# Kernel optimization log

Measured on AMD Instinct MI355X. Metric: run time of the kernel, lower is better.

## Reference

```python
import jax, jax.numpy as jnp
import numpy as np

N_FFT = 2048
HOP = 512
OUT_CH = N_FFT // 2 + 1  # 1025


def _dft_conv_weights():
    # periodic ('fftbins=True') Hann window, win_length == n_fft so no padding
    n = np.arange(N_FFT)
    window = 0.5 - 0.5 * np.cos(2.0 * np.pi * n / N_FFT)
    k = np.arange(OUT_CH)
    ang = 2.0 * np.pi * np.outer(k, n) / N_FFT  # (OUT_CH, N_FFT)
    w_real = (np.cos(ang) * window[None, :]).astype(np.float32)
    w_imag = (-np.sin(ang) * window[None, :]).astype(np.float32)
    return jnp.asarray(w_real), jnp.asarray(w_imag)


def setup_inputs() -> dict:
    key = jax.random.key(0)
    x = jax.random.normal(key, (32, 2, 160000), dtype=jnp.float32)
    W_real, W_imag = _dft_conv_weights()
    return {"x": x, "W_real": W_real, "W_imag": W_imag}


def reference(x, W_real, W_imag):
    # x: (B, C, L). center=True -> reflect pad by n_fft//2 on both sides.
    pad = N_FFT // 2
    x_pad = jnp.pad(x, ((0, 0), (0, 0), (pad, pad)), mode="reflect")
    L = x_pad.shape[-1]
    num_frames = (L - N_FFT) // HOP + 1  # 313
    # frame indices: (T, N_FFT)
    idx = jnp.arange(num_frames)[:, None] * HOP + jnp.arange(N_FFT)[None, :]
    frames = x_pad[..., idx]  # (B, C, T, N_FFT)
    # windowed DFT as matmul (equivalent to the Conv1d with stride=hop)
    real = jnp.einsum("bctn,kn->bctk", frames, W_real)
    imag = jnp.einsum("bctn,kn->bctk", frames, W_imag)
    return real, imag
```

## Files before the change

### kernel.cpp

```cpp
#include <hip/hip_runtime.h>

#define B_     32
#define C_     2
#define L_     160000
#define HOP    512
#define PAD    1024
#define LPAD   162048
#define T_     313
#define BC     64
#define M_     20032
#define KCH    1025
#define OUT_HALF 20532800UL
#define PL     81024
#define KD     1024
#define ND     1024
#define NKT    32
#define MT     157
#define NTD    8
#define NWG    1256
#define LIMW   8336

typedef __attribute__((ext_vector_type(8))) short short8;
typedef __attribute__((ext_vector_type(4))) float f32x4;

static __device__ __forceinline__ short f2bf(float f) {
  union { float f; unsigned u; } v; v.f = f;
  unsigned u = v.u;
  unsigned r = (u + 0x7fffu + ((u >> 16) & 1u)) >> 16;
  return (short)r;
}

__global__ void prep_planes(const float* __restrict__ x,
                            short* __restrict__ pl0, short* __restrict__ pl1) {
  int v = blockIdx.x * 256 + threadIdx.x;
  int bc = v / 10128;
  int r  = v - bc * 10128;
  int p0 = r * 8;
  const float* src = x + (size_t)bc * L_;
  short8 e, o;
  if (r >= 64 && r <= 10000) {
    int j0 = 16 * r - 1024;
    #pragma unroll
    for (int qq = 0; qq < 4; ++qq) {
      float4 f = *(const float4*)(src + j0 + qq * 4);
      e[qq * 2 + 0] = f2bf(f.x); o[qq * 2 + 0] = f2bf(f.y);
      e[qq * 2 + 1] = f2bf(f.z); o[qq * 2 + 1] = f2bf(f.w);
    }
  } else {
    #pragma unroll
    for (int u = 0; u < 16; ++u) {
      int j = 16 * r + u - 1024;
      j = j < 0 ? -j : j;
      j = j >= L_ ? 2 * L_ - 2 - j : j;
      short b = f2bf(src[j]);
      if (u & 1) o[u >> 1] = b; else e[u >> 1] = b;
    }
  }
  *(short8*)&pl0[(size_t)bc * PL + p0] = e;
  *(short8*)&pl1[(size_t)bc * PL + p0] = o;
}

__global__ void prep_wb(short* __restrict__ wb0, short* __restrict__ wb1) {
  int id = blockIdx.x * 256 + threadIdx.x;
  int s   = id >> 17;
  int row = (id >> 7) & 1023;
  int n8  = (id & 127) * 8;
  int kp  = row >> 1, e = row & 1;
  short8 ov;
  #pragma unroll
  for (int u = 0; u < 8; ++u) {
    int n1 = n8 + u;
    float win = 0.5f - 0.5f * cosf((float)(2 * n1 + s) * 3.0679615757712823e-3f);
    float tw;
    if (e == 0)       tw = cosf((float)((n1 * kp) & 1023) * 6.1359231515425649e-3f);
    else if (kp == 0) tw = (n1 & 1) ? -1.0f : 1.0f;
    else              tw = -sinf((float)((n1 * kp) & 1023) * 6.1359231515425649e-3f);
    ov[u] = f2bf(win * tw);
  }
  short* wb = s ? wb1 : wb0;
  *(short8*)&wb[(size_t)row * KD + n8] = ov;
}

#define GLOAD16(g, l) __builtin_amdgcn_global_load_lds(                        \
    (const __attribute__((address_space(1))) void*)(g),                        \
    (__attribute__((address_space(3))) void*)(l), 16, 0, 0)

__global__ __launch_bounds__(256, 2) void stft_gemm(const short* __restrict__ pl0,
                                                    const short* __restrict__ pl1,
                                                    const short* __restrict__ wb0,
                                                    const short* __restrict__ wb1,
                                                    float* __restrict__ out) {
  __shared__ __align__(16) char lds[66688];
  const int tid  = threadIdx.x;
  const int lane = tid & 63;
  const int wid  = tid >> 6;

  const int nt = blockIdx.x & 7;
  const int mt = blockIdx.x >> 3;
  const int M0 = mt * 128, N0 = nt * 128;

  const int chunkSwz = ((tid & 3) ^ ((tid >> 3) & 3)) * 8;
  const short* aP[2][2];
  const short* bP[2][2];
  #pragma unroll
  for (int j = 0; j < 2; ++j) {
    int row = j * 64 + (tid >> 2);
    int m = M0 + row; if (m > M_ - 1) m = M_ - 1;
    int bc = m / T_;
    int t  = m - bc * T_;
    size_t base = (size_t)bc * PL + (size_t)t * 256 + chunkSwz;
    aP[0][j] = pl0 + base;
    aP[1][j] = pl1 + base;
    size_t bb = (size_t)(N0 + row) * KD + chunkSwz;
    bP[0][j] = wb0 + bb;
    bP[1][j] = wb1 + bb;
  }
  const int dst[2] = { 0 * 4096 + tid * 16, 1 * 4096 + tid * 16 };

  const int wr = wid >> 1, wc = wid & 1;
  const int fr = lane & 15;
  const int xorb = ((lane >> 4) * 16) ^ ((fr & 6) << 3);
  int afOff[2][4], bfOff[2][4];
  #pragma unroll
  for (int i = 0; i < 4; ++i) {
    afOff[0][i] = (wr * 64 + i * 16 + fr) * 64 + xorb;
    afOff[1][i] = 8192 + (wr * 64 + i * 16 + fr) * 64 + xorb;
    bfOff[0][i] = 16384 + (wc * 64 + i * 16 + fr) * 64 + xorb;
    bfOff[1][i] = 24576 + (wc * 64 + i * 16 + fr) * 64 + xorb;
  }

  f32x4 acc[2][4][4];
  #pragma unroll
  for (int s = 0; s < 2; ++s)
    #pragma unroll
    for (int i = 0; i < 4; ++i)
      #pragma unroll
      for (int j = 0; j < 4; ++j) acc[s][i][j] = (f32x4){0.f, 0.f, 0.f, 0.f};

  {
    char* buf = lds;
    GLOAD16(aP[0][0], buf + dst[0]);
    GLOAD16(aP[0][1], buf + dst[1]);
    GLOAD16(bP[0][0], buf + 16384 + dst[0]);
    GLOAD16(bP[0][1], buf + 16384 + dst[1]);
    GLOAD16(aP[1][0], buf + 8192 + dst[0]);
    GLOAD16(aP[1][1], buf + 8192 + dst[1]);
    GLOAD16(bP[1][0], buf + 24576 + dst[0]);
    GLOAD16(bP[1][1], buf + 24576 + dst[1]);
  }

  for (int kt = 0; kt < NKT; ++kt) {
    char* bufR = lds + (kt & 1) * 32768;
    char* bufW = lds + ((kt + 1) & 1) * 32768;
    const int kos = (kt + 1) * 32;
    const bool st = (kt < NKT - 1);

    asm volatile("s_waitcnt vmcnt(4)" ::: "memory");
    __builtin_amdgcn_s_barrier();
    if (st) {
      GLOAD16(aP[0][0] + kos, bufW + dst[0]);
      GLOAD16(aP[0][1] + kos, bufW + dst[1]);
      GLOAD16(bP[0][0] + kos, bufW + 16384 + dst[0]);
      GLOAD16(bP[0][1] + kos, bufW + 16384 + dst[1]);
    }
    short8 af0[4], bf0[4];
    #pragma unroll
    for (int i = 0; i < 4; ++i) af0[i] = *(const short8*)(bufR + afOff[0][i]);
    #pragma unroll
    for (int i = 0; i < 4; ++i) bf0[i] = *(const short8*)(bufR + bfOff[0][i]);
    __builtin_amdgcn_s_barrier();
    __builtin_amdgcn_s_setprio(1);
    #pragma unroll
    for (int i = 0; i < 4; ++i)
      #pragma unroll
      for (int j = 0; j < 4; ++j)
        acc[0][i][j] = __builtin_amdgcn_mfma_f32_16x16x32_bf16(af0[i], bf0[j],
                                                               acc[0][i][j], 0, 0, 0);
    __builtin_amdgcn_s_setprio(0);

    if (st) asm volatile("s_waitcnt vmcnt(4)" ::: "memory");
    else    asm volatile("s_waitcnt vmcnt(0)" ::: "memory");
    __builtin_amdgcn_s_barrier();
    if (st) {
      GLOAD16(aP[1][0] + kos, bufW + 8192 + dst[0]);
      GLOAD16(aP[1][1] + kos, bufW + 8192 + dst[1]);
      GLOAD16(bP[1][0] + kos, bufW + 24576 + dst[0]);
      GLOAD16(bP[1][1] + kos, bufW + 24576 + dst[1]);
    }
    short8 af1[4], bf1[4];
    #pragma unroll
    for (int i = 0; i < 4; ++i) af1[i] = *(const short8*)(bufR + afOff[1][i]);
    #pragma unroll
    for (int i = 0; i < 4; ++i) bf1[i] = *(const short8*)(bufR + bfOff[1][i]);
    __builtin_amdgcn_s_barrier();
    __builtin_amdgcn_s_setprio(1);
    #pragma unroll
    for (int i = 0; i < 4; ++i)
      #pragma unroll
      for (int j = 0; j < 4; ++j)
        acc[1][i][j] = __builtin_amdgcn_mfma_f32_16x16x32_bf16(af1[i], bf1[j],
                                                               acc[1][i][j], 0, 0, 0);
    __builtin_amdgcn_s_setprio(0);
  }

  float* L = (float*)lds;
  float* outI = out + OUT_HALF;
  const float PIQ = 3.0679615757712823e-3f;
  const int rgrp = (lane >> 4) << 2;

  __syncthreads();

  #pragma unroll
  for (int pass = 0; pass < 2; ++pass) {
    #pragma unroll
    for (int j = 0; j < 4; ++j) {
      int c  = wc * 64 + j * 16 + fr;
      int q  = c >> 1;
      int qg = nt * 64 + q;
      float ang = (float)qg * PIQ;
      float tr = cosf(ang), sn = sinf(ang);
      bool odd  = c & 1;
      bool spec = (nt == 0) && (c == 1);
      float sgn = odd ? -sn : sn;
      int widx = (odd ? LIMW : 0) + (pass ? (63 - q) : q);
      #pragma unroll
      for (int i = 0; i < 4; ++i) {
        int row = wr * 64 + i * 16 + rgrp;
        #pragma unroll
        for (int r = 0; r < 4; ++r) {
          float v0 = acc[0][i][j][r];
          float v1 = acc[1][i][j][r];
          float p1 = __shfl_xor(v1, 1);
          float u  = tr * v1 + sgn * p1;
          float val;
          if (pass == 0) val = v0 + u;
          else           val = odd ? -(v0 - u) : (v0 - u);
          if (spec) val = 0.f;
          L[widx + (row + r) * 65] = val;
          if (spec && pass == 0) {
            int gm = M0 + row + r;
            if (gm < M_) {
              out [(size_t)gm * KCH + 512] = v0;
              outI[(size_t)gm * KCH + 512] = -v1;
            }
          }
        }
      }
    }
    __syncthreads();
    {
      int col0 = pass ? (1024 - nt * 64 - 63) : (nt * 64);
      #pragma unroll
      for (int i2 = 0; i2 < 32; ++i2) {
        int row = wid + i2 * 4;
        int gm  = M0 + row;
        if (gm < M_) {
          size_t rb = (size_t)gm * KCH + col0 + lane;
          out [rb] = L[row * 65 + lane];
          outI[rb] = L[LIMW + row * 65 + lane];
        }
      }
    }
    __syncthreads();
  }
}

extern "C" void kernel_launch(void* const* d_in, const int* in_sizes, int n_in,
                              void* d_out, int out_size, void* d_ws, size_t ws_size,
                              hipStream_t stream) {
  const float* x = (const float*)d_in[0];
  float* out = (float*)d_out;

  short* pl0 = (short*)d_ws;
  short* pl1 = pl0 + (size_t)BC * PL;
  short* wb0 = pl1 + (size_t)BC * PL;
  short* wb1 = wb0 + (size_t)ND * KD;

  prep_planes<<<2532, 256, 0, stream>>>(x, pl0, pl1);
  prep_wb<<<1024, 256, 0, stream>>>(wb0, wb1);

  stft_gemm<<<NWG, 256, 0, stream>>>(pl0, pl1, wb0, wb1, out);
}
```

Baseline: 159.9 us.

## Use 512-thread blocks with 8 waves and remap block-to-tile order

Measured after the change: 139.1 us. -13.0%, faster.

```diff
diff --git a/kernel.cpp b/kernel.cpp
--- a/kernel.cpp
+++ b/kernel.cpp
@@ -15,9 +15,8 @@
 #define KD     1024
 #define ND     1024
 #define NKT    32
-#define MT     157
-#define NTD    8
-#define NWG    1256
+#define MTP    160
+#define NWG    1280
 #define LIMW   8336
 
 typedef __attribute__((ext_vector_type(8))) short short8;
@@ -85,7 +84,7 @@
     (const __attribute__((address_space(1))) void*)(g),                        \
     (__attribute__((address_space(3))) void*)(l), 16, 0, 0)
 
-__global__ __launch_bounds__(256, 2) void stft_gemm(const short* __restrict__ pl0,
+__global__ __launch_bounds__(512, 4) void stft_gemm(const short* __restrict__ pl0,
                                                     const short* __restrict__ pl1,
                                                     const short* __restrict__ wb0,
                                                     const short* __restrict__ wb1,
@@ -95,59 +94,54 @@
   const int lane = tid & 63;
   const int wid  = tid >> 6;
 
-  const int nt = blockIdx.x & 7;
-  const int mt = blockIdx.x >> 3;
+  const int id = blockIdx.x;
+  const int mt = (id & 7) * 20 + (id >> 6);
+  const int nt = (id >> 3) & 7;
   const int M0 = mt * 128, N0 = nt * 128;
 
+  const int srow = tid >> 2;
   const int chunkSwz = ((tid & 3) ^ ((tid >> 3) & 3)) * 8;
-  const short* aP[2][2];
-  const short* bP[2][2];
-  #pragma unroll
-  for (int j = 0; j < 2; ++j) {
-    int row = j * 64 + (tid >> 2);
-    int m = M0 + row; if (m > M_ - 1) m = M_ - 1;
+  const short* aP[2];
+  const short* bP[2];
+  {
+    int m = M0 + srow; if (m > M_ - 1) m = M_ - 1;
     int bc = m / T_;
     int t  = m - bc * T_;
     size_t base = (size_t)bc * PL + (size_t)t * 256 + chunkSwz;
-    aP[0][j] = pl0 + base;
-    aP[1][j] = pl1 + base;
-    size_t bb = (size_t)(N0 + row) * KD + chunkSwz;
-    bP[0][j] = wb0 + bb;
-    bP[1][j] = wb1 + bb;
-  }
-  const int dst[2] = { 0 * 4096 + tid * 16, 1 * 4096 + tid * 16 };
-
-  const int wr = wid >> 1, wc = wid & 1;
+    aP[0] = pl0 + base;
+    aP[1] = pl1 + base;
+    size_t bb = (size_t)(N0 + srow) * KD + chunkSwz;
+    bP[0] = wb0 + bb;
+    bP[1] = wb1 + bb;
+  }
+  const int dstOff = tid * 16;
+
+  const int wr = wid >> 2, wc = wid & 3;
   const int fr = lane & 15;
   const int xorb = ((lane >> 4) * 16) ^ ((fr & 6) << 3);
-  int afOff[2][4], bfOff[2][4];
-  #pragma unroll
-  for (int i = 0; i < 4; ++i) {
-    afOff[0][i] = (wr * 64 + i * 16 + fr) * 64 + xorb;
-    afOff[1][i] = 8192 + (wr * 64 + i * 16 + fr) * 64 + xorb;
-    bfOff[0][i] = 16384 + (wc * 64 + i * 16 + fr) * 64 + xorb;
-    bfOff[1][i] = 24576 + (wc * 64 + i * 16 + fr) * 64 + xorb;
-  }
-
-  f32x4 acc[2][4][4];
+  int afOff[2][4], bfOff[2][2];
+  #pragma unroll
+  for (int s = 0; s < 2; ++s) {
+    #pragma unroll
+    for (int i = 0; i < 4; ++i)
+      afOff[s][i] = s * 8192 + (wr * 64 + i * 16 + fr) * 64 + xorb;
+    #pragma unroll
+    for (int j = 0; j < 2; ++j)
+      bfOff[s][j] = 16384 + s * 8192 + (wc * 32 + j * 16 + fr) * 64 + xorb;
+  }
+
+  f32x4 acc[2][4][2];
   #pragma unroll
   for (int s = 0; s < 2; ++s)
     #pragma unroll
     for (int i = 0; i < 4; ++i)
       #pragma unroll
-      for (int j = 0; j < 4; ++j) acc[s][i][j] = (f32x4){0.f, 0.f, 0.f, 0.f};
-
-  {
-    char* buf = lds;
-    GLOAD16(aP[0][0], buf + dst[0]);
-    GLOAD16(aP[0][1], buf + dst[1]);
-    GLOAD16(bP[0][0], buf + 16384 + dst[0]);
-    GLOAD16(bP[0][1], buf + 16384 + dst[1]);
-    GLOAD16(aP[1][0], buf + 8192 + dst[0]);
-    GLOAD16(aP[1][1], buf + 8192 + dst[1]);
-    GLOAD16(bP[1][0], buf + 24576 + dst[0]);
-    GLOAD16(bP[1][1], buf + 24576 + dst[1]);
-  }
+      for (int j = 0; j < 2; ++j) acc[s][i][j] = (f32x4){0.f, 0.f, 0.f, 0.f};
+
+  GLOAD16(aP[0], lds + dstOff);
+  GLOAD16(bP[0], lds + 16384 + dstOff);
+  GLOAD16(aP[1], lds + 8192 + dstOff);
+  GLOAD16(bP[1], lds + 24576 + dstOff);
 
   for (int kt = 0; kt < NKT; ++kt) {
     char* bufR = lds + (kt & 1) * 32768;
@@ -155,49 +149,45 @@
     const int kos = (kt + 1) * 32;
     const bool st = (kt < NKT - 1);
 
-    asm volatile("s_waitcnt vmcnt(4)" ::: "memory");
+    asm volatile("s_waitcnt vmcnt(2)" ::: "memory");
     __builtin_amdgcn_s_barrier();
     if (st) {
-      GLOAD16(aP[0][0] + kos, bufW + dst[0]);
-      GLOAD16(aP[0][1] + kos, bufW + dst[1]);
-      GLOAD16(bP[0][0] + kos, bufW + 16384 + dst[0]);
-      GLOAD16(bP[0][1] + kos, bufW + 16384 + dst[1]);
-    }
-    short8 af0[4], bf0[4];
+      GLOAD16(aP[0] + kos, bufW + dstOff);
+      GLOAD16(bP[0] + kos, bufW + 16384 + dstOff);
+    }
+    short8 af0[4], bf0[2];
     #pragma unroll
     for (int i = 0; i < 4; ++i) af0[i] = *(const short8*)(bufR + afOff[0][i]);
     #pragma unroll
-    for (int i = 0; i < 4; ++i) bf0[i] = *(const short8*)(bufR + bfOff[0][i]);
+    for (int j = 0; j < 2; ++j) bf0[j] = *(const short8*)(bufR + bfOff[0][j]);
     __builtin_amdgcn_s_barrier();
     __builtin_amdgcn_s_setprio(1);
     #pragma unroll
     for (int i = 0; i < 4; ++i)
       #pragma unroll
-      for (int j = 0; j < 4; ++j)
+      for (int j = 0; j < 2; ++j)
         acc[0][i][j] = __builtin_amdgcn_mfma_f32_16x16x32_bf16(af0[i], bf0[j],
                                                                acc[0][i][j], 0, 0, 0);
     __builtin_amdgcn_s_setprio(0);
 
-    if (st) asm volatile("s_waitcnt vmcnt(4)" ::: "memory");
+    if (st) asm volatile("s_waitcnt vmcnt(2)" ::: "memory");
     else    asm volatile("s_waitcnt vmcnt(0)" ::: "memory");
     __builtin_amdgcn_s_barrier();
     if (st) {
-      GLOAD16(aP[1][0] + kos, bufW + 8192 + dst[0]);
-      GLOAD16(aP[1][1] + kos, bufW + 8192 + dst[1]);
-      GLOAD16(bP[1][0] + kos, bufW + 24576 + dst[0]);
-      GLOAD16(bP[1][1] + kos, bufW + 24576 + dst[1]);
-    }
-    short8 af1[4], bf1[4];
+      GLOAD16(aP[1] + kos, bufW + 8192 + dstOff);
+      GLOAD16(bP[1] + kos, bufW + 24576 + dstOff);
+    }
+    short8 af1[4], bf1[2];
     #pragma unroll
     for (int i = 0; i < 4; ++i) af1[i] = *(const short8*)(bufR + afOff[1][i]);
     #pragma unroll
-    for (int i = 0; i < 4; ++i) bf1[i] = *(const short8*)(bufR + bfOff[1][i]);
+    for (int j = 0; j < 2; ++j) bf1[j] = *(const short8*)(bufR + bfOff[1][j]);
     __builtin_amdgcn_s_barrier();
     __builtin_amdgcn_s_setprio(1);
     #pragma unroll
     for (int i = 0; i < 4; ++i)
       #pragma unroll
-      for (int j = 0; j < 4; ++j)
+      for (int j = 0; j < 2; ++j)
         acc[1][i][j] = __builtin_amdgcn_mfma_f32_16x16x32_bf16(af1[i], bf1[j],
                                                                acc[1][i][j], 0, 0, 0);
     __builtin_amdgcn_s_setprio(0);
@@ -213,8 +203,8 @@
   #pragma unroll
   for (int pass = 0; pass < 2; ++pass) {
     #pragma unroll
-    for (int j = 0; j < 4; ++j) {
-      int c  = wc * 64 + j * 16 + fr;
+    for (int j = 0; j < 2; ++j) {
+      int c  = wc * 32 + j * 16 + fr;
       int q  = c >> 1;
       int qg = nt * 64 + q;
       float ang = (float)qg * PIQ;
@@ -251,8 +241,8 @@
     {
       int col0 = pass ? (1024 - nt * 64 - 63) : (nt * 64);
       #pragma unroll
-      for (int i2 = 0; i2 < 32; ++i2) {
-        int row = wid + i2 * 4;
+      for (int i2 = 0; i2 < 16; ++i2) {
+        int row = wid + i2 * 8;
         int gm  = M0 + row;
         if (gm < M_) {
           size_t rb = (size_t)gm * KCH + col0 + lane;
@@ -279,5 +269,5 @@
   prep_planes<<<2532, 256, 0, stream>>>(x, pl0, pl1);
   prep_wb<<<1024, 256, 0, stream>>>(wb0, wb1);
 
-  stft_gemm<<<NWG, 256, 0, stream>>>(pl0, pl1, wb0, wb1, out);
-}
+  stft_gemm<<<NWG, 512, 0, stream>>>(pl0, pl1, wb0, wb1, out);
+}
```
